# Kernel optimization log

Hardware: AMD Instinct MI355X
Metric: run time of the kernel (lower is better)

Reference implementation:

```python
import jax, jax.numpy as jnp
import numpy as np

B, C, H, W = 4, 64, 64, 64
E = C // 8  # embedding_channels = inChannels // k


def _conv1x1(x, w, b):
    # x:[B,C,H,W], w:[O,C], b:[O] -> [B,O,H,W]
    return jnp.einsum('bchw,oc->bohw', x, w) + b[None, :, None, None]


def setup_inputs() -> dict:
    key = jax.random.key(0)
    ks = jax.random.split(key, 10)
    s_c = 1.0 / np.sqrt(C)
    s_e = 1.0 / np.sqrt(E)
    x = jax.random.normal(ks[0], (B, C, H, W), jnp.float32)
    Wk = jax.random.normal(ks[1], (E, C), jnp.float32) * s_c
    bk = jax.random.normal(ks[2], (E,), jnp.float32) * 0.01
    Wq = jax.random.normal(ks[3], (E, C), jnp.float32) * s_c
    bq = jax.random.normal(ks[4], (E,), jnp.float32) * 0.01
    Wv = jax.random.normal(ks[5], (E, C), jnp.float32) * s_c
    bv = jax.random.normal(ks[6], (E,), jnp.float32) * 0.01
    Wo = jax.random.normal(ks[7], (C, E), jnp.float32) * s_e
    bo = jax.random.normal(ks[8], (C,), jnp.float32) * 0.01
    gamma = jax.random.normal(ks[9], (), jnp.float32) * 0.1  # module inits to 0; randomized for nontrivial math
    return {"x": x, "Wk": Wk, "bk": bk, "Wq": Wq, "bq": bq,
            "Wv": Wv, "bv": bv, "Wo": Wo, "bo": bo, "gamma": gamma}


def reference(x, Wk, bk, Wq, bq, Wv, bv, Wo, bo, gamma):
    b, c, h, w = x.shape
    n = h * w
    f = _conv1x1(x, Wk, bk).reshape(b, E, n)  # key
    g = _conv1x1(x, Wq, bq).reshape(b, E, n)  # query
    hx = _conv1x1(x, Wv, bv).reshape(b, E, n)  # value
    # s[b,i,j] = sum_e f[b,e,i] * g[b,e,j]  (bmm(f^T, g))
    s = jnp.einsum('bei,bej->bij', f, g)
    # torch softmax over dim=1 (the f/key index i)
    beta = jax.nn.softmax(s, axis=1)
    # v[b,e,j] = sum_i hx[b,e,i] * beta[b,i,j]
    v = jnp.einsum('bei,bij->bej', hx, beta).reshape(b, E, h, w)
    o = _conv1x1(v, Wo, bo)
    y = gamma * o + x
    y = jnp.where(y >= 0, y, 0.01 * y)  # LeakyReLU(0.01)
    return (y, beta)
```

## Files before the change

kernel.cpp:

```cpp
#include <hip/hip_runtime.h>


namespace {
constexpr int Bb = 4;
constexpr int Cc = 64;
constexpr int Nn = 4096;
constexpr int Ee = 8;
constexpr int COLS = 64;
constexpr int SPLIT_B = 4;
constexpr int CHUNK_B = Nn / SPLIT_B;
constexpr int WB = 8;
constexpr int ISB = CHUNK_B / WB;
constexpr int VPT = 4;
constexpr int TC = 256;
constexpr int JBLK = TC * VPT;
constexpr int JQ = Nn / JBLK;
constexpr int ITILE = 32;
constexpr int SI = Nn / ITILE;
constexpr float LOG2E = 1.4426950408889634f;
}

typedef float f4v __attribute__((ext_vector_type(4)));

#if defined(__has_builtin)
#if __has_builtin(__builtin_amdgcn_exp2f)
#define EXP2F(x) __builtin_amdgcn_exp2f(x)
#endif
#endif
#ifndef EXP2F
#define EXP2F(x) exp2f(x)
#endif

__global__ __launch_bounds__(256) void proj_kernel(
    const float* __restrict__ x,
    const float* __restrict__ Wk, const float* __restrict__ bk,
    const float* __restrict__ Wq, const float* __restrict__ bq,
    const float* __restrict__ Wv, const float* __restrict__ bv,
    float* __restrict__ fo, float* __restrict__ go, float* __restrict__ ho)
{
    __shared__ float wk[Ee * Cc], wq[Ee * Cc], wv[Ee * Cc];
    __shared__ float sb[3 * Ee];
    const int t = threadIdx.x;
    for (int i = t; i < Ee * Cc; i += 256) { wk[i] = Wk[i]; wq[i] = Wq[i]; wv[i] = Wv[i]; }
    if (t < Ee) { sb[t] = bk[t]; sb[Ee + t] = bq[t]; sb[2 * Ee + t] = bv[t]; }
    __syncthreads();

    const int gidx = blockIdx.x * 256 + t;
    const int b = gidx >> 12;
    const int n = gidx & (Nn - 1);

    float af[Ee], ag[Ee], ah[Ee];
#pragma unroll
    for (int e = 0; e < Ee; e++) { af[e] = sb[e]; ag[e] = sb[Ee + e]; ah[e] = sb[2 * Ee + e]; }

    const float* xp = x + (size_t)b * Cc * Nn + n;
#pragma unroll 4
    for (int c = 0; c < Cc; c++) {
        const float xv = xp[(size_t)c * Nn];
#pragma unroll
        for (int e = 0; e < Ee; e++) {
            af[e] = fmaf(wk[e * Cc + c], xv, af[e]);
            ag[e] = fmaf(wq[e * Cc + c], xv, ag[e]);
            ah[e] = fmaf(wv[e * Cc + c], xv, ah[e]);
        }
    }
    float4* fp = (float4*)(fo + (size_t)gidx * Ee);
    float4* gp = (float4*)(go + (size_t)gidx * Ee);
    float4* hp = (float4*)(ho + (size_t)gidx * Ee);
    fp[0] = make_float4(af[0], af[1], af[2], af[3]);
    fp[1] = make_float4(af[4], af[5], af[6], af[7]);
    gp[0] = make_float4(ag[0], ag[1], ag[2], ag[3]);
    gp[1] = make_float4(ag[4], ag[5], ag[6], ag[7]);
    hp[0] = make_float4(ah[0], ah[1], ah[2], ah[7 - 3]);
    hp[1] = make_float4(ah[4], ah[5], ah[6], ah[7]);
}

__global__ __launch_bounds__(512, 8) void sumv_kernel(
    const float* __restrict__ f, const float* __restrict__ g,
    const float* __restrict__ h,
    float* __restrict__ sums_part, float* __restrict__ v_part)
{
    const int b = blockIdx.x >> 8;
    const int jbase = ((blockIdx.x >> 2) & 63) * COLS;
    const int si = blockIdx.x & 3;
    const int t = threadIdx.x;
    const int lane = t & 63;
    const int w = __builtin_amdgcn_readfirstlane(t >> 6);
    const int j = jbase + lane;

    const float4* gp = (const float4*)(g + ((size_t)b * Nn + j) * Ee);
    const float4 g0 = gp[0], g1 = gp[1];
    const float gq[Ee] = {g0.x * LOG2E, g0.y * LOG2E, g0.z * LOG2E, g0.w * LOG2E,
                          g1.x * LOG2E, g1.y * LOG2E, g1.z * LOG2E, g1.w * LOG2E};

    const float* fb = f + (size_t)b * Nn * Ee;
    const float* hb = h + (size_t)b * Nn * Ee;
    const int i0 = si * CHUNK_B + w * ISB;

    float sum = 0.f;
    float vacc[Ee] = {};
#pragma unroll 4
    for (int ii = 0; ii < ISB; ii++) {
        const int i = i0 + ii;
        const float4* fr = (const float4*)(fb + (size_t)i * Ee);
        const float4 a0 = fr[0], a1 = fr[1];
        float sA = a0.x * gq[0];
        sA = fmaf(a0.y, gq[1], sA); sA = fmaf(a0.z, gq[2], sA); sA = fmaf(a0.w, gq[3], sA);
        float sB = a1.x * gq[4];
        sB = fmaf(a1.y, gq[5], sB); sB = fmaf(a1.z, gq[6], sB); sB = fmaf(a1.w, gq[7], sB);
        const float e = EXP2F(sA + sB);
        sum += e;
        const float4* hr = (const float4*)(hb + (size_t)i * Ee);
        const float4 h0 = hr[0], h1 = hr[1];
        vacc[0] = fmaf(h0.x, e, vacc[0]); vacc[1] = fmaf(h0.y, e, vacc[1]);
        vacc[2] = fmaf(h0.z, e, vacc[2]); vacc[3] = fmaf(h0.w, e, vacc[3]);
        vacc[4] = fmaf(h1.x, e, vacc[4]); vacc[5] = fmaf(h1.y, e, vacc[5]);
        vacc[6] = fmaf(h1.z, e, vacc[6]); vacc[7] = fmaf(h1.w, e, vacc[7]);
    }

    __shared__ float red[WB][COLS];
    __shared__ float vred[WB][COLS][Ee];
    red[w][lane] = sum;
    float4* vw = (float4*)&vred[w][lane][0];
    vw[0] = make_float4(vacc[0], vacc[1], vacc[2], vacc[3]);
    vw[1] = make_float4(vacc[4], vacc[5], vacc[6], vacc[7]);
    __syncthreads();
    if (t < COLS) {
        float sf = 0.f;
#pragma unroll
        for (int ww = 0; ww < WB; ww++) sf += red[ww][t];
        sums_part[(size_t)si * (Bb * Nn) + (size_t)b * Nn + jbase + t] = sf;
    }
    {
        const int col = t >> 3;
        const int e = t & 7;
        float acc = 0.f;
#pragma unroll
        for (int ww = 0; ww < WB; ww++) acc += vred[ww][col][e];
        v_part[(size_t)si * (Bb * Nn * Ee) +
               ((size_t)b * Nn + jbase + col) * Ee + e] = acc;
    }
}

__global__ __launch_bounds__(TC, 8) void beta_kernel(
    const float* __restrict__ f, const float* __restrict__ g,
    const float* __restrict__ sums_part, float* __restrict__ beta)
{
    const int blk = blockIdx.x;
    const int b  = blk >> 9;
    const int jq = (blk >> 7) & (JQ - 1);
    const int si = blk & (SI - 1);
    const int t  = threadIdx.x;
    const int j0 = jq * JBLK + t * VPT;
    const int i0 = si * ITILE;

    __shared__ float fs[ITILE * Ee];
    const float* fb = f + (size_t)b * Nn * Ee;
    fs[t] = fb[(size_t)i0 * Ee + t];

    float gq[VPT][Ee];
    {
        const float* gp = g + ((size_t)b * Nn + j0) * Ee;
#pragma unroll
        for (int jj = 0; jj < VPT; jj++) {
            const float4 a0 = ((const float4*)(gp + jj * Ee))[0];
            const float4 a1 = ((const float4*)(gp + jj * Ee))[1];
            gq[jj][0] = a0.x * LOG2E; gq[jj][1] = a0.y * LOG2E;
            gq[jj][2] = a0.z * LOG2E; gq[jj][3] = a0.w * LOG2E;
            gq[jj][4] = a1.x * LOG2E; gq[jj][5] = a1.y * LOG2E;
            gq[jj][6] = a1.z * LOG2E; gq[jj][7] = a1.w * LOG2E;
        }
    }
    float inv[VPT];
#pragma unroll
    for (int jj = 0; jj < VPT; jj++) {
        float sf = 0.f;
#pragma unroll
        for (int s2 = 0; s2 < SPLIT_B; s2++)
            sf += sums_part[(size_t)s2 * (Bb * Nn) + (size_t)b * Nn + j0 + jj];
        inv[jj] = 1.0f / sf;
    }
    __syncthreads();

    float* bp = beta + (size_t)b * Nn * Nn + j0;
#pragma unroll 4
    for (int ii = 0; ii < ITILE; ii++) {
        const float4 a0 = ((const float4*)fs)[ii * 2];
        const float4 a1 = ((const float4*)fs)[ii * 2 + 1];
        float p[VPT];
#pragma unroll
        for (int jj = 0; jj < VPT; jj++) {
            float sA = a0.x * gq[jj][0];
            sA = fmaf(a0.y, gq[jj][1], sA);
            sA = fmaf(a0.z, gq[jj][2], sA);
            sA = fmaf(a0.w, gq[jj][3], sA);
            float sB = a1.x * gq[jj][4];
            sB = fmaf(a1.y, gq[jj][5], sB);
            sB = fmaf(a1.z, gq[jj][6], sB);
            sB = fmaf(a1.w, gq[jj][7], sB);
            p[jj] = EXP2F(sA + sB) * inv[jj];
        }
        f4v pv = {p[0], p[1], p[2], p[3]};
        *(f4v*)(bp + (size_t)(i0 + ii) * Nn) = pv;
    }
}

__global__ __launch_bounds__(256) void out_kernel(
    const float* __restrict__ v_part, const float* __restrict__ sums_part,
    const float* __restrict__ Wo, const float* __restrict__ bo,
    const float* __restrict__ x, const float* __restrict__ gamma_p,
    float* __restrict__ y)
{
    __shared__ float wo[Cc * Ee];
    __shared__ float sbo[Cc];
    const int t = threadIdx.x;
    for (int i = t; i < Cc * Ee; i += 256) wo[i] = Wo[i];
    if (t < Cc) sbo[t] = bo[t];
    __syncthreads();
    const float gamma = gamma_p[0];

    const int gidx = blockIdx.x * 256 + t;
    const int b = gidx >> 12;
    const int n = gidx & (Nn - 1);

    float sf = 0.f;
#pragma unroll
    for (int s2 = 0; s2 < SPLIT_B; s2++)
        sf += sums_part[(size_t)s2 * (Bb * Nn) + gidx];
    const float inv = 1.0f / sf;

    float vv[Ee] = {};
#pragma unroll
    for (int s2 = 0; s2 < SPLIT_B; s2++) {
        const float4* vp = (const float4*)(v_part + (size_t)s2 * (Bb * Nn * Ee) + (size_t)gidx * Ee);
        const float4 v0 = vp[0], v1 = vp[1];
        vv[0] += v0.x; vv[1] += v0.y; vv[2] += v0.z; vv[3] += v0.w;
        vv[4] += v1.x; vv[5] += v1.y; vv[6] += v1.z; vv[7] += v1.w;
    }
#pragma unroll
    for (int e = 0; e < Ee; e++) vv[e] *= inv;

    const float* xp = x + (size_t)b * Cc * Nn + n;
    float* yp = y + (size_t)b * Cc * Nn + n;
#pragma unroll 4
    for (int c = 0; c < Cc; c++) {
        float o = sbo[c];
#pragma unroll
        for (int e = 0; e < Ee; e++) o = fmaf(wo[c * Ee + e], vv[e], o);
        const float t2 = fmaf(gamma, o, xp[(size_t)c * Nn]);
        yp[(size_t)c * Nn] = (t2 >= 0.f) ? t2 : 0.01f * t2;
    }
}

extern "C" void kernel_launch(void* const* d_in, const int* in_sizes, int n_in,
                              void* d_out, int out_size, void* d_ws, size_t ws_size,
                              hipStream_t stream)
{
    const float* x     = (const float*)d_in[0];
    const float* Wk    = (const float*)d_in[1];
    const float* bk    = (const float*)d_in[2];
    const float* Wq    = (const float*)d_in[3];
    const float* bq    = (const float*)d_in[4];
    const float* Wv    = (const float*)d_in[5];
    const float* bv    = (const float*)d_in[6];
    const float* Wo    = (const float*)d_in[7];
    const float* bo    = (const float*)d_in[8];
    const float* gamma = (const float*)d_in[9];

    float* y    = (float*)d_out;
    float* beta = y + (size_t)Bb * Cc * Nn;

    float* f = (float*)d_ws;
    float* g = f + (size_t)Bb * Nn * Ee;
    float* h = g + (size_t)Bb * Nn * Ee;
    float* sums_part = h + (size_t)Bb * Nn * Ee;
    float* v_part = sums_part + (size_t)SPLIT_B * Bb * Nn;

    proj_kernel<<<Bb * Nn / 256, 256, 0, stream>>>(x, Wk, bk, Wq, bq, Wv, bv, f, g, h);
    sumv_kernel<<<Bb * (Nn / COLS) * SPLIT_B, 512, 0, stream>>>(f, g, h, sums_part, v_part);
    beta_kernel<<<Bb * JQ * SI, TC, 0, stream>>>(f, g, sums_part, beta);
    out_kernel<<<Bb * Nn / 256, 256, 0, stream>>>(v_part, sums_part, Wo, bo, x, gamma, y);
}
```

Measured before the change: 361.7 us.

## Restructure beta kernel into full-row 1024-thread blocks with folded log normalizer

Each beta block now covers a full row of 4096 j columns with 1024 threads and 32 i rows. The f values are read straight from global memory as broadcast loads, which removes the shared-memory staging and the barrier. The softmax normalizer is folded into the exponent as -log2(sum), so the per-element multiply by the inverse goes away, at the cost of a small rounding change. Blocks are fewer and larger (512 instead of 2048). A cosmetic index expression in proj_kernel is also cleaned up.

```diff
diff --git a/kernel.cpp b/kernel.cpp
--- a/kernel.cpp
+++ b/kernel.cpp
@@ -12,11 +12,8 @@
 constexpr int WB = 8;
 constexpr int ISB = CHUNK_B / WB;
 constexpr int VPT = 4;
-constexpr int TC = 256;
-constexpr int JBLK = TC * VPT;
-constexpr int JQ = Nn / JBLK;
-constexpr int ITILE = 32;
-constexpr int SI = Nn / ITILE;
+constexpr int TCW = 1024;
+constexpr int RPB = 32;
 constexpr float LOG2E = 1.4426950408889634f;
 }
 
@@ -71,7 +68,7 @@
     fp[1] = make_float4(af[4], af[5], af[6], af[7]);
     gp[0] = make_float4(ag[0], ag[1], ag[2], ag[3]);
     gp[1] = make_float4(ag[4], ag[5], ag[6], ag[7]);
-    hp[0] = make_float4(ah[0], ah[1], ah[2], ah[7 - 3]);
+    hp[0] = make_float4(ah[0], ah[1], ah[2], ah[3]);
     hp[1] = make_float4(ah[4], ah[5], ah[6], ah[7]);
 }
 
@@ -142,23 +139,17 @@
     }
 }
 
-__global__ __launch_bounds__(TC, 8) void beta_kernel(
+__global__ __launch_bounds__(TCW, 4) void beta_kernel(
     const float* __restrict__ f, const float* __restrict__ g,
     const float* __restrict__ sums_part, float* __restrict__ beta)
 {
     const int blk = blockIdx.x;
-    const int b  = blk >> 9;
-    const int jq = (blk >> 7) & (JQ - 1);
-    const int si = blk & (SI - 1);
+    const int b  = blk >> 7;
+    const int i0 = (blk & 127) * RPB;
     const int t  = threadIdx.x;
-    const int j0 = jq * JBLK + t * VPT;
-    const int i0 = si * ITILE;
-
-    __shared__ float fs[ITILE * Ee];
-    const float* fb = f + (size_t)b * Nn * Ee;
-    fs[t] = fb[(size_t)i0 * Ee + t];
-
-    float gq[VPT][Ee];
+    const int j0 = t * VPT;
+
+    float gq[VPT][Ee], cj[VPT];
     {
         const float* gp = g + ((size_t)b * Nn + j0) * Ee;
 #pragma unroll
@@ -170,23 +161,23 @@
             gq[jj][4] = a1.x * LOG2E; gq[jj][5] = a1.y * LOG2E;
             gq[jj][6] = a1.z * LOG2E; gq[jj][7] = a1.w * LOG2E;
         }
-    }
-    float inv[VPT];
-#pragma unroll
-    for (int jj = 0; jj < VPT; jj++) {
-        float sf = 0.f;
-#pragma unroll
-        for (int s2 = 0; s2 < SPLIT_B; s2++)
-            sf += sums_part[(size_t)s2 * (Bb * Nn) + (size_t)b * Nn + j0 + jj];
-        inv[jj] = 1.0f / sf;
-    }
-    __syncthreads();
-
+#pragma unroll
+        for (int jj = 0; jj < VPT; jj++) {
+            float sf = 0.f;
+#pragma unroll
+            for (int s2 = 0; s2 < SPLIT_B; s2++)
+                sf += sums_part[(size_t)s2 * (Bb * Nn) + (size_t)b * Nn + j0 + jj];
+            cj[jj] = -log2f(sf);
+        }
+    }
+
+    const float* fb = f + (size_t)b * Nn * Ee;
     float* bp = beta + (size_t)b * Nn * Nn + j0;
-#pragma unroll 4
-    for (int ii = 0; ii < ITILE; ii++) {
-        const float4 a0 = ((const float4*)fs)[ii * 2];
-        const float4 a1 = ((const float4*)fs)[ii * 2 + 1];
+#pragma unroll 2
+    for (int ii = 0; ii < RPB; ii++) {
+        const int i = i0 + ii;
+        const float4 a0 = ((const float4*)(fb + (size_t)i * Ee))[0];
+        const float4 a1 = ((const float4*)(fb + (size_t)i * Ee))[1];
         float p[VPT];
 #pragma unroll
         for (int jj = 0; jj < VPT; jj++) {
@@ -194,14 +185,14 @@
             sA = fmaf(a0.y, gq[jj][1], sA);
             sA = fmaf(a0.z, gq[jj][2], sA);
             sA = fmaf(a0.w, gq[jj][3], sA);
-            float sB = a1.x * gq[jj][4];
+            float sB = fmaf(a1.x, gq[jj][4], cj[jj]);
             sB = fmaf(a1.y, gq[jj][5], sB);
             sB = fmaf(a1.z, gq[jj][6], sB);
             sB = fmaf(a1.w, gq[jj][7], sB);
-            p[jj] = EXP2F(sA + sB) * inv[jj];
+            p[jj] = EXP2F(sA + sB);
         }
         f4v pv = {p[0], p[1], p[2], p[3]};
-        *(f4v*)(bp + (size_t)(i0 + ii) * Nn) = pv;
+        *(f4v*)(bp + (size_t)i * Nn) = pv;
     }
 }
 
@@ -278,6 +269,6 @@
 
     proj_kernel<<<Bb * Nn / 256, 256, 0, stream>>>(x, Wk, bk, Wq, bq, Wv, bv, f, g, h);
     sumv_kernel<<<Bb * (Nn / COLS) * SPLIT_B, 512, 0, stream>>>(f, g, h, sums_part, v_part);
-    beta_kernel<<<Bb * JQ * SI, TC, 0, stream>>>(f, g, sums_part, beta);
+    beta_kernel<<<Bb * (Nn / RPB), TCW, 0, stream>>>(f, g, sums_part, beta);
     out_kernel<<<Bb * Nn / 256, 256, 0, stream>>>(v_part, sums_part, Wo, bo, x, gamma, y);
 }
```

Result: no change. 358.7 us (-0.8%).
